# Kernel optimization log

Hardware: AMD Instinct MI355X
Metric: run time of the kernel (lower is better)

Reference implementation:

```python
import jax, jax.numpy as jnp
import numpy as np

EPS = 1e-5

# ---------------- numpy-side hash/index precomputation ----------------

def _key(c):
    c = c.astype(np.int64) + 2  # shift so all coords >= 0
    return (c[..., 0] * 4096 + c[..., 1]) * 4096 + c[..., 2]

def _lookup(table_keys, query_keys):
    order = np.argsort(table_keys)
    sk = table_keys[order]
    pos = np.clip(np.searchsorted(sk, query_keys), 0, len(sk) - 1)
    found = sk[pos] == query_keys
    return np.where(found, order[pos], -1).astype(np.int64)

def setup_inputs() -> dict:
    N, C_IN, C_OUT, RES = 400_000, 32, 64, 1.0
    rng = np.random.default_rng(0)
    coords = rng.uniform(0.0, 100.0, (N, 3)).astype(np.float32)
    pf = rng.standard_normal((N, C_IN)).astype(np.float32)

    # initial_voxelize: unique voxel coords + point->voxel map
    vc = np.floor(coords / RES).astype(np.int64)
    uv, p2v_in = np.unique(vc, axis=0, return_inverse=True)
    p2v_in = p2v_in.reshape(-1)
    cnt_in = np.bincount(p2v_in, minlength=len(uv)).astype(np.float32)

    # strided conv output lattice (stride 2)
    ouv = np.unique(uv // 2, axis=0)
    ikeys, okeys = _key(uv), _key(ouv)

    # kernel-2 stride-2 conv map: input voxel at 2*out + off, off in {0,1}^3
    offs2 = np.array([[i, j, k] for i in (0, 1) for j in (0, 1) for k in (0, 1)], np.int64)
    conv_map = np.stack([_lookup(ikeys, _key(ouv * 2 + o)) for o in offs2], axis=1)

    # kernel-3 neighbor map on the output lattice
    offs3 = np.array([[i, j, k] for i in (-1, 0, 1) for j in (-1, 0, 1) for k in (-1, 0, 1)], np.int64)
    nbr27 = np.stack([_lookup(okeys, _key(ouv + o)) for o in offs3], axis=1)

    # trilinear voxel_to_point on output lattice (voxel size = 2*RES)
    q = coords / (2.0 * RES)
    base = np.floor(q).astype(np.int64)
    frac = (q - base).astype(np.float32)
    tri_idx, tri_w = [], []
    for o in offs2:
        idx = _lookup(okeys, _key(base + o))
        w = np.prod(np.where(o[None, :] == 1, frac, 1.0 - frac), axis=1).astype(np.float32)
        tri_idx.append(idx)
        tri_w.append(np.where(idx >= 0, w, 0.0).astype(np.float32))
    tri_idx = np.stack(tri_idx, axis=1)
    tri_w = np.stack(tri_w, axis=1)

    # point_to_voxel: containing output voxel (always exists)
    p2v_out = _lookup(okeys, _key(base))
    cnt_out = np.bincount(p2v_out, minlength=len(ouv)).astype(np.float32)

    def glorot(r, *shape):
        fan_in = shape[-2] * int(np.prod(shape[:-2])) if len(shape) > 2 else shape[0]
        return (r.standard_normal(shape) / np.sqrt(fan_in)).astype(np.float32)

    return dict(
        pf=jnp.asarray(pf),
        Wc=jnp.asarray(glorot(rng, 8, C_IN, C_OUT)),
        g1=jnp.ones(C_OUT, jnp.float32), b1=jnp.zeros(C_OUT, jnp.float32),
        Wr1=jnp.asarray(glorot(rng, 27, C_OUT, C_OUT)),
        gr1=jnp.ones(C_OUT, jnp.float32), br1=jnp.zeros(C_OUT, jnp.float32),
        Wr2=jnp.asarray(glorot(rng, 27, C_OUT, C_OUT)),
        gr2=jnp.ones(C_OUT, jnp.float32), br2=jnp.zeros(C_OUT, jnp.float32),
        Wpt=jnp.asarray(glorot(rng, C_OUT, C_OUT)), bpt=jnp.zeros(C_OUT, jnp.float32),
        gp=jnp.ones(C_OUT, jnp.float32), bp=jnp.zeros(C_OUT, jnp.float32),
        tri_w=jnp.asarray(tri_w), cnt_in=jnp.asarray(cnt_in), cnt_out=jnp.asarray(cnt_out),
        p2v_in=jnp.asarray(p2v_in), conv_map=jnp.asarray(conv_map),
        nbr27=jnp.asarray(nbr27), tri_idx=jnp.asarray(tri_idx), p2v_out=jnp.asarray(p2v_out),
    )

# ---------------- jax forward ----------------

def _bn(x, g, b):  # training-mode batch norm over voxel/point dim
    m = x.mean(0)
    v = x.var(0)
    return (x - m) * jax.lax.rsqrt(v + EPS) * g + b

def _seg_mean(x, seg, cnt):  # spvoxelize: scatter-mean
    return jax.ops.segment_sum(x, seg, num_segments=cnt.shape[0]) / cnt[:, None]

def _sconv(f, nbr, W):  # sparse conv: per-offset gather + matmul accumulate
    out = jnp.zeros((nbr.shape[0], W.shape[2]), f.dtype)
    for k in range(W.shape[0]):
        idx = nbr[:, k]
        g = jnp.where((idx >= 0)[:, None], f[jnp.maximum(idx, 0)], 0.0)
        out = out + g @ W[k]
    return out

def _tri(f, idx, w):  # trilinear voxel->point gather (w already 0 for missing)
    out = jnp.zeros((idx.shape[0], f.shape[1]), f.dtype)
    for j in range(idx.shape[1]):
        out = out + w[:, j:j + 1] * f[jnp.maximum(idx[:, j], 0)]
    return out

def reference(pf, Wc, g1, b1, Wr1, gr1, br1, Wr2, gr2, br2, Wpt, bpt, gp, bp,
              tri_w, cnt_in, cnt_out, p2v_in, conv_map, nbr27, tri_idx, p2v_out):
    vf0 = _seg_mean(pf, p2v_in, cnt_in)                         # initial_voxelize [M_in,32]
    vf1 = jax.nn.relu(_bn(_sconv(vf0, conv_map, Wc), g1, b1))   # conv_in [M_out,64]
    pfeat = _tri(vf1, tri_idx, tri_w)                           # voxel_to_point [N,64]
    vf2 = _seg_mean(pfeat, p2v_out, cnt_out)                    # point_to_voxel [M_out,64]
    h = jax.nn.relu(_bn(_sconv(vf2, nbr27, Wr1), gr1, br1))     # ResBlock conv1
    h = jax.nn.relu(_bn(_sconv(h, nbr27, Wr2), gr2, br2))       # ResBlock conv2
    vf3 = h + vf2                                               # residual sum
    p_out = jax.nn.relu(_bn(pfeat @ Wpt + bpt, gp, bp))         # point_layer
    pfeat2 = _tri(vf3, tri_idx, tri_w) + p_out                  # v2p + fuse
    vf4 = _seg_mean(pfeat2, p2v_out, cnt_out)                   # point_to_voxel
    return vf4, pfeat2
```

## Files before the change

kernel.cpp:

```cpp
#include <hip/hip_runtime.h>

#define EPSV 1e-5f
#define CDIV(a, b) (((a) + (b) - 1) / (b))

using short8 = __attribute__((ext_vector_type(8))) short;
using f32x4 = __attribute__((ext_vector_type(4))) float;

__device__ __forceinline__ unsigned short bf16rne(float x) {
  unsigned u = __float_as_uint(x);
  unsigned r = (u + 0x7fffu + ((u >> 16) & 1u)) >> 16;
  return (unsigned short)r;
}

__global__ void k_scatter_in(const float* __restrict__ pf, const int* __restrict__ p2v,
                             float* __restrict__ vf0, int total) {
  int i = blockIdx.x * 256 + threadIdx.x;
  if (i >= total) return;
  atomicAdd(&vf0[(size_t)p2v[i >> 5] * 32 + (i & 31)], pf[i]);
}

__global__ void k_div_in(float* __restrict__ vf0, const float* __restrict__ cnt, int total) {
  int i = blockIdx.x * 256 + threadIdx.x;
  if (i >= total) return;
  vf0[i] /= cnt[i >> 5];
}

__global__ __launch_bounds__(256) void k_conv1(const float* __restrict__ vin,
                                               const int* __restrict__ cmap,
                                               const float* __restrict__ W,
                                               float* __restrict__ out,
                                               float* __restrict__ stats, int Vout) {
  __shared__ float fs[32][128];
  __shared__ float Ws[32 * 64];
  __shared__ int idxs[128 * 8];
  __shared__ float ss[128];
  const int tid = threadIdx.x;
  const int vb = blockIdx.x * 128;
  for (int i = tid; i < 128 * 8; i += 256) {
    int g = vb * 8 + i;
    idxs[i] = (g < Vout * 8) ? cmap[g] : -1;
  }
  if (tid < 128) ss[tid] = 0.f;
  const int vq = tid & 15, cq = tid >> 4;
  const int v0 = vq * 8, c0 = cq * 4;
  const int srow = tid & 127, sci = (tid >> 7) * 16;
  float acc[8][4];
#pragma unroll
  for (int r = 0; r < 8; ++r)
#pragma unroll
    for (int q = 0; q < 4; ++q) acc[r][q] = 0.f;

  for (int k = 0; k < 8; ++k) {
    __syncthreads();
    for (int i = tid; i < 32 * 64; i += 256) Ws[i] = W[k * 2048 + i];
    int idx = idxs[srow * 8 + k];
    if (idx >= 0) {
#pragma unroll
      for (int j = 0; j < 16; j += 4) {
        float4 t = *(const float4*)&vin[(size_t)idx * 32 + sci + j];
        fs[sci + j + 0][srow] = t.x;
        fs[sci + j + 1][srow] = t.y;
        fs[sci + j + 2][srow] = t.z;
        fs[sci + j + 3][srow] = t.w;
      }
    } else {
#pragma unroll
      for (int j = 0; j < 16; ++j) fs[sci + j][srow] = 0.f;
    }
    __syncthreads();
#pragma unroll 8
    for (int ci = 0; ci < 32; ++ci) {
      float4 w4 = *(const float4*)&Ws[ci * 64 + c0];
      float4 fa = *(const float4*)&fs[ci][v0];
      float4 fb = *(const float4*)&fs[ci][v0 + 4];
      float fv[8] = {fa.x, fa.y, fa.z, fa.w, fb.x, fb.y, fb.z, fb.w};
      float wv[4] = {w4.x, w4.y, w4.z, w4.w};
#pragma unroll
      for (int r = 0; r < 8; ++r)
#pragma unroll
        for (int q = 0; q < 4; ++q) acc[r][q] += fv[r] * wv[q];
    }
  }
  float s1[4] = {0, 0, 0, 0}, s2[4] = {0, 0, 0, 0};
#pragma unroll
  for (int r = 0; r < 8; ++r) {
    int v = vb + v0 + r;
    if (v < Vout) {
      *(float4*)&out[(size_t)v * 64 + c0] =
          make_float4(acc[r][0], acc[r][1], acc[r][2], acc[r][3]);
#pragma unroll
      for (int q = 0; q < 4; ++q) {
        float x = acc[r][q];
        s1[q] += x;
        s2[q] += x * x;
      }
    }
  }
#pragma unroll
  for (int q = 0; q < 4; ++q) {
    atomicAdd(&ss[c0 + q], s1[q]);
    atomicAdd(&ss[64 + c0 + q], s2[q]);
  }
  __syncthreads();
  if (tid < 128) atomicAdd(&stats[tid], ss[tid]);
}

__global__ void k_bnfin(const float* __restrict__ stats, const float* __restrict__ g,
                        const float* __restrict__ b, float* __restrict__ sb, int rows) {
  int c = threadIdx.x;
  float inv = 1.f / (float)rows;
  float m = stats[c] * inv;
  float v = stats[64 + c] * inv - m * m;
  float sc = g[c] * rsqrtf(v + EPSV);
  sb[c] = sc;
  sb[64 + c] = b[c] - m * sc;
}

__global__ __launch_bounds__(1024) void k_scan_part(const float* __restrict__ cnt,
                                                    int* __restrict__ partial, int V) {
  __shared__ int s[1024];
  int i = blockIdx.x * 1024 + threadIdx.x;
  s[threadIdx.x] = (i < V) ? (int)cnt[i] : 0;
  __syncthreads();
  for (int st = 512; st > 0; st >>= 1) {
    if (threadIdx.x < st) s[threadIdx.x] += s[threadIdx.x + st];
    __syncthreads();
  }
  if (threadIdx.x == 0) partial[blockIdx.x] = s[0];
}

__global__ __launch_bounds__(1024) void k_scan_top(int* __restrict__ partial, int nb) {
  __shared__ int s[1024];
  int t = threadIdx.x;
  int orig = (t < nb) ? partial[t] : 0;
  s[t] = orig;
  __syncthreads();
  for (int st = 1; st < 1024; st <<= 1) {
    int v = (t >= st) ? s[t - st] : 0;
    __syncthreads();
    s[t] += v;
    __syncthreads();
  }
  if (t < nb) partial[t] = s[t] - orig;
}

__global__ __launch_bounds__(1024) void k_scan_write(const float* __restrict__ cnt,
                                                     const int* __restrict__ partial,
                                                     int* __restrict__ starts,
                                                     int* __restrict__ cursor, int V) {
  __shared__ int s[1024];
  int t = threadIdx.x;
  int i = blockIdx.x * 1024 + t;
  int orig = (i < V) ? (int)cnt[i] : 0;
  s[t] = orig;
  __syncthreads();
  for (int st = 1; st < 1024; st <<= 1) {
    int v = (t >= st) ? s[t - st] : 0;
    __syncthreads();
    s[t] += v;
    __syncthreads();
  }
  if (i < V) {
    int excl = s[t] - orig + partial[blockIdx.x];
    starts[i] = excl;
    cursor[i] = excl;
  }
}

__global__ void k_bucket(const int* __restrict__ p2v, int* __restrict__ cursor,
                         int* __restrict__ plist, int N) {
  int p = blockIdx.x * 256 + threadIdx.x;
  if (p >= N) return;
  int pos = atomicAdd(&cursor[p2v[p]], 1);
  plist[pos] = p;
}

__global__ __launch_bounds__(256) void k_tri1v(const float* __restrict__ c1,
                                               const float* __restrict__ sb0,
                                               const int* __restrict__ tidx,
                                               const float* __restrict__ twt,
                                               const int* __restrict__ starts,
                                               const float* __restrict__ cnt,
                                               const int* __restrict__ plist,
                                               float* __restrict__ pfeat,
                                               float* __restrict__ vf2, int V) {
  int t = threadIdx.x;
  int v = blockIdx.x * 4 + (t >> 6);
  int c = t & 63;
  if (v >= V) return;
  int s0 = starts[v];
  int n = (int)cnt[v];
  if (n < 1) return;
  int p0 = plist[s0];
  float sc = sb0[c], bi = sb0[64 + c];
  float R[8];
#pragma unroll
  for (int j = 0; j < 8; ++j) {
    int idx = tidx[(size_t)p0 * 8 + j];
    R[j] = (idx >= 0) ? fmaxf(sc * c1[(size_t)idx * 64 + c] + bi, 0.f) : 0.f;
  }
  float acc_v = 0.f;
  for (int i = 0; i < n; ++i) {
    int p = plist[s0 + i];
    float4 w0 = *(const float4*)&twt[(size_t)p * 8];
    float4 w1 = *(const float4*)&twt[(size_t)p * 8 + 4];
    float acc = w0.x * R[0] + w0.y * R[1] + w0.z * R[2] + w0.w * R[3] +
                w1.x * R[4] + w1.y * R[5] + w1.z * R[6] + w1.w * R[7];
    pfeat[(size_t)p * 64 + c] = acc;
    acc_v += acc;
  }
  vf2[(size_t)v * 64 + c] = acc_v / (float)n;
}

__global__ void k_wprep(const float* __restrict__ W, short* __restrict__ Wh,
                        short* __restrict__ Wl, int ntap) {
  int t = blockIdx.x * 256 + threadIdx.x;
  int total = ntap * 2 * 4 * 64;
  if (t >= total) return;
  int l = t & 63;
  int n = (t >> 6) & 3;
  int s = (t >> 8) & 1;
  int k = t >> 9;
  int co = n * 16 + (l & 15);
  int ci0 = s * 32 + (l >> 4) * 8;
#pragma unroll
  for (int j = 0; j < 8; ++j) {
    float x = W[((size_t)(k * 64 + ci0 + j)) * 64 + co];
    unsigned short hb = bf16rne(x);
    float hf = __uint_as_float((unsigned)hb << 16);
    Wh[(size_t)t * 8 + j] = (short)hb;
    Wl[(size_t)t * 8 + j] = (short)bf16rne(x - hf);
  }
}

__global__ void k_split(const float* __restrict__ in, const float* __restrict__ sb,
                        short* __restrict__ oh, short* __restrict__ ol, int total) {
  int i = blockIdx.x * 256 + threadIdx.x;
  if (i >= total) return;
  float x = in[i];
  if (sb) {
    int c = i & 63;
    x = fmaxf(sb[c] * x + sb[64 + c], 0.f);
  }
  unsigned short hb = bf16rne(x);
  float hf = __uint_as_float((unsigned)hb << 16);
  oh[i] = (short)hb;
  ol[i] = (short)bf16rne(x - hf);
}

__global__ __launch_bounds__(256) void k_conv27m(const short* __restrict__ Ah_g,
                                                 const short* __restrict__ Al_g,
                                                 const int* __restrict__ nbr,
                                                 const short* __restrict__ Wh,
                                                 const short* __restrict__ Wl,
                                                 float* __restrict__ out,
                                                 float* __restrict__ stats, int Vout) {
  __shared__ alignas(16) short As_h[4 * 2 * 512];
  __shared__ alignas(16) short As_l[4 * 2 * 512];
  __shared__ int idxs[64 * 27];
  __shared__ float ss[128];
  const int tid = threadIdx.x;
  const int vb = blockIdx.x * 64;
  for (int i = tid; i < 64 * 27; i += 256) {
    int g = vb * 27 + i;
    idxs[i] = (g < Vout * 27) ? nbr[g] : -1;
  }
  if (tid < 128) ss[tid] = 0.f;
  const int lane = tid & 63;
  const int w = tid >> 6;
  f32x4 acc[4];
#pragma unroll
  for (int n = 0; n < 4; ++n)
#pragma unroll
    for (int r = 0; r < 4; ++r) acc[n][r] = 0.f;
  __syncthreads();

  for (int k = 0; k < 27; ++k) {
#pragma unroll
    for (int it = 0; it < 4; ++it) {
      int c = it * 256 + tid;
      int cc = c & 511;
      int v = cc >> 3;
      int j = cc & 7;
      int idx = idxs[v * 27 + k];
      const short* src = (c >> 9) ? Al_g : Ah_g;
      short* dst = (c >> 9) ? As_l : As_h;
      int s = j >> 2, kq = j & 3;
      int off = (((v >> 4) * 2 + s) * 512 + (kq * 16 + (v & 15)) * 8);
      uint4 val = make_uint4(0u, 0u, 0u, 0u);
      if (idx >= 0) val = *(const uint4*)&src[(size_t)idx * 64 + j * 8];
      *(uint4*)&dst[off] = val;
    }
    __syncthreads();
#pragma unroll
    for (int s = 0; s < 2; ++s) {
      short8 ah = *(const short8*)&As_h[(w * 2 + s) * 512 + lane * 8];
      short8 al = *(const short8*)&As_l[(w * 2 + s) * 512 + lane * 8];
      const short* bph = Wh + ((size_t)(k * 2 + s) * 4) * 512;
      const short* bpl = Wl + ((size_t)(k * 2 + s) * 4) * 512;
#pragma unroll
      for (int n = 0; n < 4; ++n) {
        short8 bh = *(const short8*)&bph[n * 512 + lane * 8];
        short8 bl = *(const short8*)&bpl[n * 512 + lane * 8];
        acc[n] = __builtin_amdgcn_mfma_f32_16x16x32_bf16(ah, bh, acc[n], 0, 0, 0);
        acc[n] = __builtin_amdgcn_mfma_f32_16x16x32_bf16(al, bh, acc[n], 0, 0, 0);
        acc[n] = __builtin_amdgcn_mfma_f32_16x16x32_bf16(ah, bl, acc[n], 0, 0, 0);
      }
    }
    __syncthreads();
  }

  const int col = lane & 15, rq = lane >> 4;
#pragma unroll
  for (int n = 0; n < 4; ++n) {
    int c = n * 16 + col;
    float s1 = 0.f, s2 = 0.f;
#pragma unroll
    for (int r = 0; r < 4; ++r) {
      int v = vb + w * 16 + rq * 4 + r;
      if (v < Vout) {
        float x = acc[n][r];
        out[(size_t)v * 64 + c] = x;
        s1 += x;
        s2 += x * x;
      }
    }
    atomicAdd(&ss[c], s1);
    atomicAdd(&ss[64 + c], s2);
  }
  __syncthreads();
  if (tid < 128) atomicAdd(&stats[tid], ss[tid]);
}

__global__ void k_vf3(const float* __restrict__ h2, const float* __restrict__ vf2,
                      const float* __restrict__ sb2, float* __restrict__ vf3, int total) {
  int i = blockIdx.x * 256 + threadIdx.x;
  if (i >= total) return;
  int c = i & 63;
  vf3[i] = fmaxf(sb2[c] * h2[i] + sb2[64 + c], 0.f) + vf2[i];
}

__global__ __launch_bounds__(256) void k_pmm(const float* __restrict__ pfeat,
                                             const float* __restrict__ Wpt,
                                             const float* __restrict__ bpt,
                                             float* __restrict__ outbuf,
                                             float* __restrict__ stats, int N) {
  __shared__ float fs[64][128];
  __shared__ float Ws[64 * 64];
  __shared__ float ss[128];
  const int tid = threadIdx.x;
  const int pb = blockIdx.x * 128;
  for (int i = tid; i < 64 * 64; i += 256) Ws[i] = Wpt[i];
  if (tid < 128) ss[tid] = 0.f;
  const int srow = tid & 127, sci = (tid >> 7) * 32;
  int p = pb + srow;
  if (p < N) {
#pragma unroll
    for (int j = 0; j < 32; j += 4) {
      float4 t = *(const float4*)&pfeat[(size_t)p * 64 + sci + j];
      fs[sci + j + 0][srow] = t.x;
      fs[sci + j + 1][srow] = t.y;
      fs[sci + j + 2][srow] = t.z;
      fs[sci + j + 3][srow] = t.w;
    }
  } else {
#pragma unroll
    for (int j = 0; j < 32; ++j) fs[sci + j][srow] = 0.f;
  }
  __syncthreads();
  const int vq = tid & 15, cq = tid >> 4;
  const int p0 = vq * 8, c0 = cq * 4;
  float acc[8][4];
#pragma unroll
  for (int r = 0; r < 8; ++r)
#pragma unroll
    for (int q = 0; q < 4; ++q) acc[r][q] = 0.f;
#pragma unroll 8
  for (int ci = 0; ci < 64; ++ci) {
    float4 w4 = *(const float4*)&Ws[ci * 64 + c0];
    float4 fa = *(const float4*)&fs[ci][p0];
    float4 fb = *(const float4*)&fs[ci][p0 + 4];
    float fv[8] = {fa.x, fa.y, fa.z, fa.w, fb.x, fb.y, fb.z, fb.w};
    float wv[4] = {w4.x, w4.y, w4.z, w4.w};
#pragma unroll
    for (int r = 0; r < 8; ++r)
#pragma unroll
      for (int q = 0; q < 4; ++q) acc[r][q] += fv[r] * wv[q];
  }
  float bb[4] = {bpt[c0], bpt[c0 + 1], bpt[c0 + 2], bpt[c0 + 3]};
  float s1[4] = {0, 0, 0, 0}, s2[4] = {0, 0, 0, 0};
#pragma unroll
  for (int r = 0; r < 8; ++r) {
    int pp = pb + p0 + r;
    if (pp < N) {
      float4 o;
      o.x = acc[r][0] + bb[0];
      o.y = acc[r][1] + bb[1];
      o.z = acc[r][2] + bb[2];
      o.w = acc[r][3] + bb[3];
      *(float4*)&outbuf[(size_t)pp * 64 + c0] = o;
      s1[0] += o.x; s2[0] += o.x * o.x;
      s1[1] += o.y; s2[1] += o.y * o.y;
      s1[2] += o.z; s2[2] += o.z * o.z;
      s1[3] += o.w; s2[3] += o.w * o.w;
    }
  }
#pragma unroll
  for (int q = 0; q < 4; ++q) {
    atomicAdd(&ss[c0 + q], s1[q]);
    atomicAdd(&ss[64 + c0 + q], s2[q]);
  }
  __syncthreads();
  if (tid < 128) atomicAdd(&stats[tid], ss[tid]);
}

__global__ __launch_bounds__(256) void k_tri2v(const float* __restrict__ vf3,
                                               const float* __restrict__ sb3,
                                               const int* __restrict__ tidx,
                                               const float* __restrict__ twt,
                                               const int* __restrict__ starts,
                                               const float* __restrict__ cnt,
                                               const int* __restrict__ plist,
                                               float* __restrict__ pf2,
                                               float* __restrict__ vf4, int V) {
  int t = threadIdx.x;
  int v = blockIdx.x * 4 + (t >> 6);
  int c = t & 63;
  if (v >= V) return;
  int s0 = starts[v];
  int n = (int)cnt[v];
  if (n < 1) return;
  int p0 = plist[s0];
  float S[8];
#pragma unroll
  for (int j = 0; j < 8; ++j) {
    int idx = tidx[(size_t)p0 * 8 + j];
    S[j] = (idx >= 0) ? vf3[(size_t)idx * 64 + c] : 0.f;
  }
  float s3 = sb3[c], b3 = sb3[64 + c];
  float acc_v = 0.f;
  for (int i = 0; i < n; ++i) {
    int p = plist[s0 + i];
    float4 w0 = *(const float4*)&twt[(size_t)p * 8];
    float4 w1 = *(const float4*)&twt[(size_t)p * 8 + 4];
    float raw = pf2[(size_t)p * 64 + c];
    float val = fmaxf(s3 * raw + b3, 0.f) +
                w0.x * S[0] + w0.y * S[1] + w0.z * S[2] + w0.w * S[3] +
                w1.x * S[4] + w1.y * S[5] + w1.z * S[6] + w1.w * S[7];
    pf2[(size_t)p * 64 + c] = val;
    acc_v += val;
  }
  vf4[(size_t)v * 64 + c] = acc_v / (float)n;
}

extern "C" void kernel_launch(void* const* d_in, const int* in_sizes, int n_in,
                              void* d_out, int out_size, void* d_ws, size_t ws_size,
                              hipStream_t stream) {
  const float* pf = (const float*)d_in[0];
  const float* Wc = (const float*)d_in[1];
  const float* g1 = (const float*)d_in[2];
  const float* b1 = (const float*)d_in[3];
  const float* Wr1 = (const float*)d_in[4];
  const float* gr1 = (const float*)d_in[5];
  const float* br1 = (const float*)d_in[6];
  const float* Wr2 = (const float*)d_in[7];
  const float* gr2 = (const float*)d_in[8];
  const float* br2 = (const float*)d_in[9];
  const float* Wpt = (const float*)d_in[10];
  const float* bpt = (const float*)d_in[11];
  const float* gp = (const float*)d_in[12];
  const float* bp = (const float*)d_in[13];
  const float* twt = (const float*)d_in[14];
  const float* cnt_in = (const float*)d_in[15];
  const float* cnt_out = (const float*)d_in[16];
  const int* p2v_in = (const int*)d_in[17];
  const int* conv_map = (const int*)d_in[18];
  const int* nbr27 = (const int*)d_in[19];
  const int* tri_idx = (const int*)d_in[20];
  const int* p2v_out = (const int*)d_in[21];

  const int N = in_sizes[0] / 32;
  const int Vin = in_sizes[15];
  const int Vout = in_sizes[16];

  float* ws = (float*)d_ws;
  size_t o = 0;
  auto alloc = [&](size_t nf) {
    float* pbase = ws + o;
    o += (nf + 63) & ~(size_t)63;
    return pbase;
  };
  size_t vf0_sz = (size_t)Vin * 32;
  size_t vf3_sz = (size_t)Vout * 64;
  float* vf0 = alloc(vf0_sz > vf3_sz ? vf0_sz : vf3_sz);
  float* c1 = alloc((size_t)Vout * 64);
  float* pfeat = alloc((size_t)N * 64);
  float* vf2 = alloc((size_t)Vout * 64);
  float* h1 = alloc((size_t)Vout * 64);
  float* stats = alloc(512);
  float* sb = alloc(512);
  int* partial = (int*)alloc(1024);
  int* starts = (int*)alloc(Vout);
  int* cursor = (int*)alloc(Vout);
  int* plist = (int*)alloc(N);
  const int WFRAG = 27 * 2 * 4 * 64 * 8;
  short* Wh1 = (short*)alloc(WFRAG / 2);
  short* Wl1 = (short*)alloc(WFRAG / 2);
  short* Wh2 = (short*)alloc(WFRAG / 2);
  short* Wl2 = (short*)alloc(WFRAG / 2);
  float* vf3 = vf0;
  float* h2 = c1;
  short* vf2h = (short*)pfeat;
  short* vf2l = vf2h + (size_t)Vout * 64;
  short* h1rh = vf2l + (size_t)Vout * 64;
  short* h1rl = h1rh + (size_t)Vout * 64;

  float* vf4 = (float*)d_out;
  float* pf2 = vf4 + (size_t)Vout * 64;

  const int nb = CDIV(Vout, 1024);

  hipMemsetAsync(vf0, 0, (size_t)Vin * 32 * sizeof(float), stream);
  hipMemsetAsync(stats, 0, 512 * sizeof(float), stream);

  k_scatter_in<<<CDIV(N * 32, 256), 256, 0, stream>>>(pf, p2v_in, vf0, N * 32);
  k_div_in<<<CDIV(Vin * 32, 256), 256, 0, stream>>>(vf0, cnt_in, Vin * 32);
  k_conv1<<<CDIV(Vout, 128), 256, 0, stream>>>(vf0, conv_map, Wc, c1, stats, Vout);
  k_bnfin<<<1, 64, 0, stream>>>(stats, g1, b1, sb, Vout);

  k_scan_part<<<nb, 1024, 0, stream>>>(cnt_out, partial, Vout);
  k_scan_top<<<1, 1024, 0, stream>>>(partial, nb);
  k_scan_write<<<nb, 1024, 0, stream>>>(cnt_out, partial, starts, cursor, Vout);
  k_bucket<<<CDIV(N, 256), 256, 0, stream>>>(p2v_out, cursor, plist, N);

  k_wprep<<<CDIV(27 * 2 * 4 * 64, 256), 256, 0, stream>>>(Wr1, Wh1, Wl1, 27);
  k_wprep<<<CDIV(27 * 2 * 4 * 64, 256), 256, 0, stream>>>(Wr2, Wh2, Wl2, 27);

  k_tri1v<<<CDIV(Vout, 4), 256, 0, stream>>>(c1, sb, tri_idx, twt, starts, cnt_out,
                                             plist, pfeat, vf2, Vout);

  k_pmm<<<CDIV(N, 128), 256, 0, stream>>>(pfeat, Wpt, bpt, pf2, stats + 384, N);
  k_bnfin<<<1, 64, 0, stream>>>(stats + 384, gp, bp, sb + 384, N);

  k_split<<<CDIV(Vout * 64, 256), 256, 0, stream>>>(vf2, nullptr, vf2h, vf2l, Vout * 64);
  k_conv27m<<<CDIV(Vout, 64), 256, 0, stream>>>(vf2h, vf2l, nbr27, Wh1, Wl1, h1,
                                                stats + 128, Vout);
  k_bnfin<<<1, 64, 0, stream>>>(stats + 128, gr1, br1, sb + 128, Vout);

  k_split<<<CDIV(Vout * 64, 256), 256, 0, stream>>>(h1, sb + 128, h1rh, h1rl, Vout * 64);
  k_conv27m<<<CDIV(Vout, 64), 256, 0, stream>>>(h1rh, h1rl, nbr27, Wh2, Wl2, h2,
                                                stats + 256, Vout);
  k_bnfin<<<1, 64, 0, stream>>>(stats + 256, gr2, br2, sb + 256, Vout);

  k_vf3<<<CDIV(Vout * 64, 256), 256, 0, stream>>>(h2, vf2, sb + 256, vf3, Vout * 64);

  k_tri2v<<<CDIV(Vout, 4), 256, 0, stream>>>(vf3, sb + 384, tri_idx, twt, starts,
                                             cnt_out, plist, pf2, vf4, Vout);
}
```

Measured before the change: 1.390 ms.

## Double the conv27 voxel tile and prefetch next-offset gathers into registers

The 27-neighbour MFMA convolution now handles 128 voxels per block instead of 64, so each wave computes two 16-row tiles that share the same weight fragment loads. The gather for offset k+1 is issued into registers before the MFMAs for offset k and written to shared memory after them, overlapping global gather latency with compute. This raises register and LDS use per block and halves the number of blocks, which may reduce occupancy and load balance.

```diff
diff --git a/kernel.cpp b/kernel.cpp
--- a/kernel.cpp
+++ b/kernel.cpp
@@ -255,78 +255,113 @@
                                                  const short* __restrict__ Wl,
                                                  float* __restrict__ out,
                                                  float* __restrict__ stats, int Vout) {
-  __shared__ alignas(16) short As_h[4 * 2 * 512];
-  __shared__ alignas(16) short As_l[4 * 2 * 512];
-  __shared__ int idxs[64 * 27];
+  __shared__ alignas(16) short As_h[1024 * 8];
+  __shared__ alignas(16) short As_l[1024 * 8];
+  __shared__ int idxs[128 * 27];
   __shared__ float ss[128];
   const int tid = threadIdx.x;
-  const int vb = blockIdx.x * 64;
-  for (int i = tid; i < 64 * 27; i += 256) {
+  const int vb = blockIdx.x * 128;
+  for (int i = tid; i < 128 * 27; i += 256) {
     int g = vb * 27 + i;
     idxs[i] = (g < Vout * 27) ? nbr[g] : -1;
   }
   if (tid < 128) ss[tid] = 0.f;
   const int lane = tid & 63;
   const int w = tid >> 6;
-  f32x4 acc[4];
-#pragma unroll
-  for (int n = 0; n < 4; ++n)
-#pragma unroll
-    for (int r = 0; r < 4; ++r) acc[n][r] = 0.f;
+  int sv[4], sj[4];
+#pragma unroll
+  for (int it = 0; it < 4; ++it) {
+    int g = it * 256 + tid;
+    sv[it] = ((g >> 7) << 4) | (g & 15);
+    sj[it] = (g >> 4) & 7;
+  }
+  f32x4 acc[2][4];
+#pragma unroll
+  for (int m = 0; m < 2; ++m)
+#pragma unroll
+    for (int n = 0; n < 4; ++n)
+#pragma unroll
+      for (int r = 0; r < 4; ++r) acc[m][n][r] = 0.f;
+  __syncthreads();
+
+  uint4 rg[8];
+#pragma unroll
+  for (int it = 0; it < 8; ++it) {
+    int idx = idxs[sv[it & 3] * 27 + 0];
+    const short* src = (it < 4) ? Ah_g : Al_g;
+    rg[it] = (idx >= 0) ? *(const uint4*)&src[(size_t)idx * 64 + sj[it & 3] * 8]
+                        : make_uint4(0u, 0u, 0u, 0u);
+  }
+#pragma unroll
+  for (int it = 0; it < 8; ++it) {
+    int g = (it & 3) * 256 + tid;
+    short* dst = (it < 4) ? As_h : As_l;
+    *(uint4*)&dst[g * 8] = rg[it];
+  }
   __syncthreads();
 
   for (int k = 0; k < 27; ++k) {
-#pragma unroll
-    for (int it = 0; it < 4; ++it) {
-      int c = it * 256 + tid;
-      int cc = c & 511;
-      int v = cc >> 3;
-      int j = cc & 7;
-      int idx = idxs[v * 27 + k];
-      const short* src = (c >> 9) ? Al_g : Ah_g;
-      short* dst = (c >> 9) ? As_l : As_h;
-      int s = j >> 2, kq = j & 3;
-      int off = (((v >> 4) * 2 + s) * 512 + (kq * 16 + (v & 15)) * 8);
-      uint4 val = make_uint4(0u, 0u, 0u, 0u);
-      if (idx >= 0) val = *(const uint4*)&src[(size_t)idx * 64 + j * 8];
-      *(uint4*)&dst[off] = val;
-    }
-    __syncthreads();
+    if (k + 1 < 27) {
+#pragma unroll
+      for (int it = 0; it < 8; ++it) {
+        int idx = idxs[sv[it & 3] * 27 + (k + 1)];
+        const short* src = (it < 4) ? Ah_g : Al_g;
+        rg[it] = (idx >= 0) ? *(const uint4*)&src[(size_t)idx * 64 + sj[it & 3] * 8]
+                            : make_uint4(0u, 0u, 0u, 0u);
+      }
+    }
 #pragma unroll
     for (int s = 0; s < 2; ++s) {
-      short8 ah = *(const short8*)&As_h[(w * 2 + s) * 512 + lane * 8];
-      short8 al = *(const short8*)&As_l[(w * 2 + s) * 512 + lane * 8];
+      short8 ah0 = *(const short8*)&As_h[((w * 4 + s) * 64 + lane) * 8];
+      short8 al0 = *(const short8*)&As_l[((w * 4 + s) * 64 + lane) * 8];
+      short8 ah1 = *(const short8*)&As_h[((w * 4 + 2 + s) * 64 + lane) * 8];
+      short8 al1 = *(const short8*)&As_l[((w * 4 + 2 + s) * 64 + lane) * 8];
       const short* bph = Wh + ((size_t)(k * 2 + s) * 4) * 512;
       const short* bpl = Wl + ((size_t)(k * 2 + s) * 4) * 512;
 #pragma unroll
       for (int n = 0; n < 4; ++n) {
         short8 bh = *(const short8*)&bph[n * 512 + lane * 8];
         short8 bl = *(const short8*)&bpl[n * 512 + lane * 8];
-        acc[n] = __builtin_amdgcn_mfma_f32_16x16x32_bf16(ah, bh, acc[n], 0, 0, 0);
-        acc[n] = __builtin_amdgcn_mfma_f32_16x16x32_bf16(al, bh, acc[n], 0, 0, 0);
-        acc[n] = __builtin_amdgcn_mfma_f32_16x16x32_bf16(ah, bl, acc[n], 0, 0, 0);
+        acc[0][n] = __builtin_amdgcn_mfma_f32_16x16x32_bf16(ah0, bh, acc[0][n], 0, 0, 0);
+        acc[0][n] = __builtin_amdgcn_mfma_f32_16x16x32_bf16(al0, bh, acc[0][n], 0, 0, 0);
+        acc[0][n] = __builtin_amdgcn_mfma_f32_16x16x32_bf16(ah0, bl, acc[0][n], 0, 0, 0);
+        acc[1][n] = __builtin_amdgcn_mfma_f32_16x16x32_bf16(ah1, bh, acc[1][n], 0, 0, 0);
+        acc[1][n] = __builtin_amdgcn_mfma_f32_16x16x32_bf16(al1, bh, acc[1][n], 0, 0, 0);
+        acc[1][n] = __builtin_amdgcn_mfma_f32_16x16x32_bf16(ah1, bl, acc[1][n], 0, 0, 0);
       }
     }
     __syncthreads();
+    if (k + 1 < 27) {
+#pragma unroll
+      for (int it = 0; it < 8; ++it) {
+        int g = (it & 3) * 256 + tid;
+        short* dst = (it < 4) ? As_h : As_l;
+        *(uint4*)&dst[g * 8] = rg[it];
+      }
+      __syncthreads();
+    }
   }
 
   const int col = lane & 15, rq = lane >> 4;
 #pragma unroll
-  for (int n = 0; n < 4; ++n) {
-    int c = n * 16 + col;
-    float s1 = 0.f, s2 = 0.f;
-#pragma unroll
-    for (int r = 0; r < 4; ++r) {
-      int v = vb + w * 16 + rq * 4 + r;
-      if (v < Vout) {
-        float x = acc[n][r];
-        out[(size_t)v * 64 + c] = x;
-        s1 += x;
-        s2 += x * x;
+  for (int m = 0; m < 2; ++m) {
+#pragma unroll
+    for (int n = 0; n < 4; ++n) {
+      int c = n * 16 + col;
+      float s1 = 0.f, s2 = 0.f;
+#pragma unroll
+      for (int r = 0; r < 4; ++r) {
+        int v = vb + w * 32 + m * 16 + rq * 4 + r;
+        if (v < Vout) {
+          float x = acc[m][n][r];
+          out[(size_t)v * 64 + c] = x;
+          s1 += x;
+          s2 += x * x;
+        }
       }
-    }
-    atomicAdd(&ss[c], s1);
-    atomicAdd(&ss[64 + c], s2);
+      atomicAdd(&ss[c], s1);
+      atomicAdd(&ss[64 + c], s2);
+    }
   }
   __syncthreads();
   if (tid < 128) atomicAdd(&stats[tid], ss[tid]);
@@ -543,13 +578,13 @@
   k_bnfin<<<1, 64, 0, stream>>>(stats + 384, gp, bp, sb + 384, N);
 
   k_split<<<CDIV(Vout * 64, 256), 256, 0, stream>>>(vf2, nullptr, vf2h, vf2l, Vout * 64);
-  k_conv27m<<<CDIV(Vout, 64), 256, 0, stream>>>(vf2h, vf2l, nbr27, Wh1, Wl1, h1,
-                                                stats + 128, Vout);
+  k_conv27m<<<CDIV(Vout, 128), 256, 0, stream>>>(vf2h, vf2l, nbr27, Wh1, Wl1, h1,
+                                                 stats + 128, Vout);
   k_bnfin<<<1, 64, 0, stream>>>(stats + 128, gr1, br1, sb + 128, Vout);
 
   k_split<<<CDIV(Vout * 64, 256), 256, 0, stream>>>(h1, sb + 128, h1rh, h1rl, Vout * 64);
-  k_conv27m<<<CDIV(Vout, 64), 256, 0, stream>>>(h1rh, h1rl, nbr27, Wh2, Wl2, h2,
-                                                stats + 256, Vout);
+  k_conv27m<<<CDIV(Vout, 128), 256, 0, stream>>>(h1rh, h1rl, nbr27, Wh2, Wl2, h2,
+                                                 stats + 256, Vout);
   k_bnfin<<<1, 64, 0, stream>>>(stats + 256, gr2, br2, sb + 256, Vout);
 
   k_vf3<<<CDIV(Vout * 64, 256), 256, 0, stream>>>(h2, vf2, sb + 256, vf3, Vout * 64);
```

Result: no change. 1.399 ms (+0.7%).
